# Kernel optimization log

Measured on AMD Instinct MI355X. Metric: run time of the kernel, lower is better.

## Reference

```python
import jax, jax.numpy as jnp
import numpy as np

N = 100000      # nodes
E = 1200000     # edges
D_IN = 128      # input_dim
H = 64          # hidden_dim
OUT = 3         # output_dim
EPS = 1e-5      # BatchNorm eps


def setup_inputs() -> dict:
    key = jax.random.key(0)
    ks = jax.random.split(key, 24)
    w = lambda k, shape: jax.random.normal(k, shape, jnp.float32) * 0.05
    return {
        "x": jax.random.normal(ks[0], (N, D_IN), jnp.float32),
        "edge_index": jax.random.randint(ks[1], (2, E), 0, N, dtype=jnp.int32),
        "proj_W": w(ks[2], (H, D_IN)), "proj_b": w(ks[3], (H,)),
        "conv1_W": w(ks[4], (H, H)), "conv1_b": w(ks[5], (H,)),
        "bn1_g": jnp.ones((H,), jnp.float32), "bn1_b": w(ks[6], (H,)),
        "conv2_W": w(ks[7], (H, H)), "conv2_b": w(ks[8], (H,)),
        "bn2_g": jnp.ones((H,), jnp.float32), "bn2_b": w(ks[9], (H,)),
        "conv3_W": w(ks[10], (H, H)), "conv3_b": w(ks[11], (H,)),
        "bn3_g": jnp.ones((H,), jnp.float32), "bn3_b": w(ks[12], (H,)),
        "byp_W": w(ks[13], (OUT, D_IN)), "byp_b": w(ks[14], (OUT,)),
        "head_W": w(ks[15], (OUT, H + OUT)), "head_b": w(ks[16], (OUT,)),
    }


def reference(x, edge_index, proj_W, proj_b,
              conv1_W, conv1_b, bn1_g, bn1_b,
              conv2_W, conv2_b, bn2_g, bn2_b,
              conv3_W, conv3_b, bn3_g, bn3_b,
              byp_W, byp_b, head_W, head_b):
    n = x.shape[0]
    row, col = edge_index[0], edge_index[1]
    loop = jnp.arange(n, dtype=row.dtype)
    row_f = jnp.concatenate([row, loop])   # source (with self loops)
    col_f = jnp.concatenate([col, loop])   # target
    # symmetric GCN normalization: deg over targets of A+I, edge weight 1
    deg = jax.ops.segment_sum(jnp.ones(row_f.shape, jnp.float32), col_f, num_segments=n)
    dinv = jnp.where(deg > 0, jax.lax.rsqrt(deg), 0.0)
    norm = dinv[row_f] * dinv[col_f]       # [E+N]

    def gcn(h, W, b):
        h = h @ W.T                                    # transform then propagate
        msg = h[row_f] * norm[:, None]                 # gather + scale
        return jax.ops.segment_sum(msg, col_f, num_segments=n) + b

    def bn(h, g, b):
        # eval-mode BatchNorm1d: running_mean=0, running_var=1 buffers
        return h * (g / jnp.sqrt(1.0 + EPS)) + b

    h = x @ proj_W.T + proj_b
    idn = h
    h = jax.nn.relu(bn(gcn(h, conv1_W, conv1_b), bn1_g, bn1_b)) + idn  # dropout inactive (eval)
    idn = h
    h = jax.nn.relu(bn(gcn(h, conv2_W, conv2_b), bn2_g, bn2_b)) + idn
    h = jax.nn.relu(bn(gcn(h, conv3_W, conv3_b), bn3_g, bn3_b))

    byp = x @ byp_W.T + byp_b
    p = jnp.concatenate([h, byp], axis=1) @ head_W.T + head_b
    kappa = jnp.clip(p[:, 0] * 5.0 + 2.5, 0.2, 10.0)
    alpha = p[:, 1]
    tau = jnp.clip(p[:, 2] + 0.5, 0.05, 2.0)
    return jnp.stack([kappa, alpha, tau], axis=1)
```

## Files before the change

kernel.cpp:

```cpp
#include <hip/hip_runtime.h>
#include <hip/hip_fp16.h>

#define NN 100000
#define NE 1200000
#define NBUK ((NN + 127) / 128)
#define NCHUNK 512

typedef _Float16 h8 __attribute__((ext_vector_type(8)));
typedef float f32x4 __attribute__((ext_vector_type(4)));
typedef float f32x2 __attribute__((ext_vector_type(2)));

__global__ __launch_bounds__(256) void k_bucketA(const int* __restrict__ col,
                                                 int* __restrict__ blkcnt,
                                                 int* __restrict__ bcnt) {
    __shared__ int lh[NBUK];
    const int tid = threadIdx.x;
    const int per = (NE + NCHUNK - 1) / NCHUNK;
    const int e0 = blockIdx.x * per;
    const int e1 = (e0 + per < NE) ? (e0 + per) : NE;
    for (int i = tid; i < NBUK; i += 256) lh[i] = 0;
    __syncthreads();
    for (int e = e0 + tid; e < e1; e += 256)
        atomicAdd(&lh[col[e] >> 7], 1);
    __syncthreads();
    for (int b = tid; b < NBUK; b += 256) {
        int v = lh[b];
        blkcnt[b * NCHUNK + blockIdx.x] = v;
        if (v) atomicAdd(&bcnt[b], v);
    }
}

__global__ __launch_bounds__(1024) void k_scanAll(int* __restrict__ blkcnt,
                                                  int* __restrict__ bcnt) {
    __shared__ int s[1024];
    const int b = blockIdx.x, tid = threadIdx.x;
    if (b < NBUK) {
        int v = (tid < NCHUNK) ? blkcnt[b * NCHUNK + tid] : 0;
        s[tid] = v;
        __syncthreads();
        #pragma unroll
        for (int d = 1; d < 1024; d <<= 1) {
            int t = (tid >= d) ? s[tid - d] : 0;
            __syncthreads();
            s[tid] += t;
            __syncthreads();
        }
        if (tid < NCHUNK) blkcnt[b * NCHUNK + tid] = s[tid] - v;
    } else {
        int v = (tid < NBUK) ? bcnt[tid] : 0;
        s[tid] = v;
        __syncthreads();
        #pragma unroll
        for (int d = 1; d < 1024; d <<= 1) {
            int t = (tid >= d) ? s[tid - d] : 0;
            __syncthreads();
            s[tid] += t;
            __syncthreads();
        }
        if (tid < NBUK) bcnt[tid] = s[tid] - v;
        if (tid == 0) bcnt[NBUK] = NE;
    }
}

__global__ __launch_bounds__(256) void k_bucketB(const int* __restrict__ row,
                                                 const int* __restrict__ col,
                                                 const int* __restrict__ bbase,
                                                 const int* __restrict__ blkcnt,
                                                 unsigned* __restrict__ tmp) {
    __shared__ int lh[NBUK];
    const int tid = threadIdx.x;
    const int per = (NE + NCHUNK - 1) / NCHUNK;
    const int e0 = blockIdx.x * per;
    const int e1 = (e0 + per < NE) ? (e0 + per) : NE;
    for (int b = tid; b < NBUK; b += 256)
        lh[b] = bbase[b] + blkcnt[b * NCHUNK + blockIdx.x];
    __syncthreads();
    for (int e = e0 + tid; e < e1; e += 256) {
        int c = col[e], r = row[e];
        int pos = atomicAdd(&lh[c >> 7], 1);
        tmp[pos] = ((unsigned)r << 7) | (unsigned)(c & 127);
    }
}

__global__ __launch_bounds__(256) void k_build(const unsigned* __restrict__ tmp,
                                               const int* __restrict__ bbase,
                                               int* __restrict__ off,
                                               float* __restrict__ dinv,
                                               int* __restrict__ csr_row) {
    __shared__ int cnt[128], s[128], cur[128];
    const int b = blockIdx.x, tid = threadIdx.x;
    const int colBase = b << 7;
    const int nCols = (NN - colBase < 128) ? (NN - colBase) : 128;
    const int seg0 = bbase[b], seg1 = bbase[b + 1];
    if (tid < 128) cnt[tid] = 0;
    __syncthreads();
    for (int i = seg0 + tid; i < seg1; i += 256)
        atomicAdd(&cnt[tmp[i] & 127], 1);
    __syncthreads();
    if (tid < 128) s[tid] = cnt[tid];
    __syncthreads();
    #pragma unroll
    for (int d = 1; d < 128; d <<= 1) {
        int t = (tid < 128 && tid >= d) ? s[tid - d] : 0;
        __syncthreads();
        if (tid < 128) s[tid] += t;
        __syncthreads();
    }
    if (tid < nCols) {
        int exc = seg0 + s[tid] - cnt[tid];
        off[colBase + tid] = exc;
        cur[tid] = exc;
        dinv[colBase + tid] = rsqrtf((float)cnt[tid] + 1.0f);
    }
    if (b == 0 && tid == 0) off[NN] = NE;
    __syncthreads();
    for (int i = seg0 + tid; i < seg1; i += 256) {
        unsigned v = tmp[i];
        int pos = atomicAdd(&cur[v & 127u], 1);
        csr_row[pos] = (int)(v >> 7);
    }
}

__global__ __launch_bounds__(256) void k_gemmPC(const float* __restrict__ X,
                                                const float* __restrict__ W,
                                                const float* __restrict__ bias,
                                                _Float16* __restrict__ Yh,
                                                const float* __restrict__ bypW,
                                                const float* __restrict__ bypb,
                                                float* __restrict__ bypOut,
                                                const float* __restrict__ convW1,
                                                const float* __restrict__ dinv,
                                                unsigned char* __restrict__ Y8,
                                                int n_nodes) {
    constexpr int D = 128, RS = D + 8, KS = D / 32;
    constexpr int RS2 = 72;
    __shared__ _Float16 Xh[64 * RS];
    __shared__ _Float16 Wh[64 * RS];
    const int tid = threadIdx.x;
    const int n0 = blockIdx.x * 64;

    for (int i = tid; i < 64 * (D / 8); i += 256) {
        int j = i / (D / 8), d8 = (i % (D / 8)) * 8;
        const float4* wp = (const float4*)&W[j * D + d8];
        float4 w0 = wp[0], w1 = wp[1];
        h8 h = { (_Float16)w0.x, (_Float16)w0.y, (_Float16)w0.z, (_Float16)w0.w,
                 (_Float16)w1.x, (_Float16)w1.y, (_Float16)w1.z, (_Float16)w1.w };
        *(h8*)&Wh[j * RS + d8] = h;
    }
    for (int i = tid; i < 64 * (D / 8); i += 256) {
        int nl = i / (D / 8), d8 = (i % (D / 8)) * 8;
        int n = n0 + nl; if (n >= n_nodes) n = n_nodes - 1;
        const float4* xp = (const float4*)&X[(size_t)n * D + d8];
        float4 x0 = xp[0], x1 = xp[1];
        h8 h = { (_Float16)x0.x, (_Float16)x0.y, (_Float16)x0.z, (_Float16)x0.w,
                 (_Float16)x1.x, (_Float16)x1.y, (_Float16)x1.z, (_Float16)x1.w };
        *(h8*)&Xh[nl * RS + d8] = h;
    }
    __syncthreads();

    const int wid = tid >> 6, lane = tid & 63;
    const int lm = lane & 15, lq = lane >> 4;
    const int mBase = wid * 16;

    h8 bfrag[4][KS];
    #pragma unroll
    for (int t = 0; t < 4; ++t)
        #pragma unroll
        for (int s = 0; s < KS; ++s)
            bfrag[t][s] = *(const h8*)&Wh[(t * 16 + lm) * RS + s * 32 + lq * 8];

    h8 bfragB[KS];
    #pragma unroll
    for (int s = 0; s < KS; ++s) {
        if (lm < 3) {
            const float4* wp = (const float4*)&bypW[lm * D + s * 32 + lq * 8];
            float4 w0 = wp[0], w1 = wp[1];
            bfragB[s] = (h8){ (_Float16)w0.x, (_Float16)w0.y, (_Float16)w0.z, (_Float16)w0.w,
                              (_Float16)w1.x, (_Float16)w1.y, (_Float16)w1.z, (_Float16)w1.w };
        } else {
            bfragB[s] = (h8)(_Float16)0;
        }
    }

    f32x4 acc[5] = {};
    #pragma unroll
    for (int s = 0; s < KS; ++s) {
        h8 a = *(const h8*)&Xh[(mBase + lm) * RS + s * 32 + lq * 8];
        #pragma unroll
        for (int t = 0; t < 4; ++t)
            acc[t] = __builtin_amdgcn_mfma_f32_16x16x32_f16(a, bfrag[t][s], acc[t], 0, 0, 0);
        acc[4] = __builtin_amdgcn_mfma_f32_16x16x32_f16(a, bfragB[s], acc[4], 0, 0, 0);
    }

    float bb[4];
    #pragma unroll
    for (int t = 0; t < 4; ++t) bb[t] = bias[t * 16 + lm];
    float bypbv = (lm < 3) ? bypb[lm] : 0.f;
    const int nodeBase = n0 + mBase + lq * 4;

    __syncthreads();

    #pragma unroll
    for (int r = 0; r < 4; ++r) {
        int node = nodeBase + r;
        int nloc = mBase + lq * 4 + r;
        #pragma unroll
        for (int t = 0; t < 4; ++t) {
            _Float16 hv = (_Float16)(acc[t][r] + bb[t]);
            Xh[nloc * RS2 + t * 16 + lm] = hv;
            if (node < n_nodes)
                Yh[(size_t)node * 64 + t * 16 + lm] = hv;
        }
        if (node < n_nodes && lm < 3)
            bypOut[node * 3 + lm] = acc[4][r] + bypbv;
    }
    for (int i = tid; i < 64 * 8; i += 256) {
        int j = i >> 3, d8 = (i & 7) * 8;
        const float4* wp = (const float4*)&convW1[j * 64 + d8];
        float4 w0 = wp[0], w1 = wp[1];
        h8 h = { (_Float16)w0.x, (_Float16)w0.y, (_Float16)w0.z, (_Float16)w0.w,
                 (_Float16)w1.x, (_Float16)w1.y, (_Float16)w1.z, (_Float16)w1.w };
        *(h8*)&Wh[j * RS2 + d8] = h;
    }
    __syncthreads();

    h8 cfrag[4][2];
    #pragma unroll
    for (int t = 0; t < 4; ++t)
        #pragma unroll
        for (int s = 0; s < 2; ++s)
            cfrag[t][s] = *(const h8*)&Wh[(t * 16 + lm) * RS2 + s * 32 + lq * 8];

    f32x4 acc2[4] = {};
    #pragma unroll
    for (int s = 0; s < 2; ++s) {
        h8 a = *(const h8*)&Xh[(mBase + lm) * RS2 + s * 32 + lq * 8];
        #pragma unroll
        for (int t = 0; t < 4; ++t)
            acc2[t] = __builtin_amdgcn_mfma_f32_16x16x32_f16(a, cfrag[t][s], acc2[t], 0, 0, 0);
    }
    #pragma unroll
    for (int r = 0; r < 4; ++r) {
        int node = nodeBase + r;
        if (node < n_nodes) {
            float sdv = dinv[node];
            #pragma unroll
            for (int t = 0; t < 4; ++t) {
                float v = acc2[t][r] * sdv;
                int pk = __builtin_amdgcn_cvt_pk_fp8_f32(v, v, 0, false);
                Y8[(size_t)node * 64 + t * 16 + lm] = (unsigned char)(pk & 0xff);
            }
        }
    }
}

__device__ __forceinline__ void acc_fp8(float* acc, uint2 w) {
    f32x2 p0 = __builtin_amdgcn_cvt_pk_f32_fp8(w.x, false);
    f32x2 p1 = __builtin_amdgcn_cvt_pk_f32_fp8(w.x, true);
    f32x2 p2 = __builtin_amdgcn_cvt_pk_f32_fp8(w.y, false);
    f32x2 p3 = __builtin_amdgcn_cvt_pk_f32_fp8(w.y, true);
    acc[0] += p0.x; acc[1] += p0.y; acc[2] += p1.x; acc[3] += p1.y;
    acc[4] += p2.x; acc[5] += p2.y; acc[6] += p3.x; acc[7] += p3.y;
}

template<bool HEAD>
__global__ __launch_bounds__(256) void k_gather(const unsigned char* __restrict__ hB8,
                                                const float* __restrict__ dinv,
                                                const int* __restrict__ off,
                                                const int* __restrict__ csr_row,
                                                const float* __restrict__ convb,
                                                const float* __restrict__ bng,
                                                const float* __restrict__ bnb,
                                                _Float16* __restrict__ hA,
                                                const float* __restrict__ nextW,
                                                unsigned char* __restrict__ Y8,
                                                const float* __restrict__ byp,
                                                const float* __restrict__ headW,
                                                const float* __restrict__ headb,
                                                float* __restrict__ out) {
    constexpr int RS2 = 72;
    __shared__ _Float16 Ws[HEAD ? 1 : 64 * RS2];
    __shared__ _Float16 Hs[HEAD ? 1 : 32 * RS2];
    __shared__ float HWs[HEAD ? 204 : 1];
    const int tid = threadIdx.x;
    if constexpr (HEAD) {
        for (int i = tid; i < 204; i += 256)
            HWs[i] = (i < 201) ? headW[i] : headb[i - 201];
        __syncthreads();
    } else {
        for (int i = tid; i < 64 * 8; i += 256) {
            int j = i >> 3, d8 = (i & 7) * 8;
            const float4* wp = (const float4*)&nextW[j * 64 + d8];
            float4 w0 = wp[0], w1 = wp[1];
            h8 h = { (_Float16)w0.x, (_Float16)w0.y, (_Float16)w0.z, (_Float16)w0.w,
                     (_Float16)w1.x, (_Float16)w1.y, (_Float16)w1.z, (_Float16)w1.w };
            *(h8*)&Ws[j * RS2 + d8] = h;
        }
    }
    const int wid = tid >> 6, lane = tid & 63;
    const int nloc = wid * 8 + (lane >> 3);
    const int n = blockIdx.x * 32 + nloc;
    const int oct = lane & 7;
    const int f0 = oct * 8;

    const int e0 = off[n];
    const int deg = off[n + 1] - e0;

    const uint2* rows8 = (const uint2*)hB8;
    float acc[8] = {0, 0, 0, 0, 0, 0, 0, 0};
    acc_fp8(acc, rows8[(size_t)n * 8 + oct]);

    for (int it = 0; it < deg; it += 8) {
        const int rem = deg - it;
        uint2 w[8];
        #pragma unroll
        for (int q = 0; q < 8; ++q) {
            int rq = csr_row[e0 + it + ((q < rem) ? q : 0)];
            w[q] = rows8[(size_t)rq * 8 + oct];
            if (q >= rem) { w[q].x = 0; w[q].y = 0; }
        }
        #pragma unroll
        for (int q = 0; q < 8; ++q)
            acc_fp8(acc, w[q]);
    }

    const float dv = dinv[n];
    const float bnscale = rsqrtf(1.0f + 1e-5f);
    const float4 cb0 = *(const float4*)&convb[f0], cb1 = *(const float4*)&convb[f0 + 4];
    const float4 g0  = *(const float4*)&bng[f0],  g1  = *(const float4*)&bng[f0 + 4];
    const float4 b0_ = *(const float4*)&bnb[f0],  b1_ = *(const float4*)&bnb[f0 + 4];
    const float cb[8] = { cb0.x, cb0.y, cb0.z, cb0.w, cb1.x, cb1.y, cb1.z, cb1.w };
    const float gg[8] = { g0.x, g0.y, g0.z, g0.w, g1.x, g1.y, g1.z, g1.w };
    const float bb[8] = { b0_.x, b0_.y, b0_.z, b0_.w, b1_.x, b1_.y, b1_.z, b1_.w };
    float v[8];
    #pragma unroll
    for (int j = 0; j < 8; ++j)
        v[j] = fmaxf((acc[j] * dv + cb[j]) * (gg[j] * bnscale) + bb[j], 0.0f);

    if constexpr (!HEAD) {
        size_t o = ((size_t)n << 6) + f0;
        h8 old = *(const h8*)&hA[o];
        #pragma unroll
        for (int j = 0; j < 8; ++j) v[j] += (float)old[j];
        h8 res = { (_Float16)v[0], (_Float16)v[1], (_Float16)v[2], (_Float16)v[3],
                   (_Float16)v[4], (_Float16)v[5], (_Float16)v[6], (_Float16)v[7] };
        *(h8*)&hA[o] = res;
        *(h8*)&Hs[nloc * RS2 + f0] = res;
        __syncthreads();

        const int lm = lane & 15, lq = lane >> 4;
        const int mt = (wid & 1) * 16;
        const int nt = (wid >> 1) * 32;
        h8 afrag[2], bfrag[2][2];
        #pragma unroll
        for (int s = 0; s < 2; ++s)
            afrag[s] = *(const h8*)&Hs[(mt + lm) * RS2 + s * 32 + lq * 8];
        #pragma unroll
        for (int t = 0; t < 2; ++t)
            #pragma unroll
            for (int s = 0; s < 2; ++s)
                bfrag[t][s] = *(const h8*)&Ws[(nt + t * 16 + lm) * RS2 + s * 32 + lq * 8];
        f32x4 acc2[2] = {};
        #pragma unroll
        for (int s = 0; s < 2; ++s)
            #pragma unroll
            for (int t = 0; t < 2; ++t)
                acc2[t] = __builtin_amdgcn_mfma_f32_16x16x32_f16(afrag[s], bfrag[t][s], acc2[t], 0, 0, 0);
        const int nodeBase = blockIdx.x * 32 + mt + lq * 4;
        #pragma unroll
        for (int r = 0; r < 4; ++r) {
            int node = nodeBase + r;
            float sdv = dinv[node];
            #pragma unroll
            for (int t = 0; t < 2; ++t) {
                float vv = acc2[t][r] * sdv;
                int pk = __builtin_amdgcn_cvt_pk_fp8_f32(vv, vv, 0, false);
                Y8[(size_t)node * 64 + nt + t * 16 + lm] = (unsigned char)(pk & 0xff);
            }
        }
    } else {
        float p[3];
        #pragma unroll
        for (int o = 0; o < 3; ++o) {
            float t = 0.f;
            #pragma unroll
            for (int j = 0; j < 8; ++j) t += v[j] * HWs[o * 67 + f0 + j];
            p[o] = t;
        }
        #pragma unroll
        for (int mask = 1; mask < 8; mask <<= 1) {
            #pragma unroll
            for (int o = 0; o < 3; ++o) p[o] += __shfl_xor(p[o], mask, 64);
        }
        if (oct == 0) {
            float by0 = byp[n * 3], by1 = byp[n * 3 + 1], by2 = byp[n * 3 + 2];
            #pragma unroll
            for (int o = 0; o < 3; ++o)
                p[o] += by0 * HWs[o * 67 + 64] + by1 * HWs[o * 67 + 65] + by2 * HWs[o * 67 + 66]
                      + HWs[201 + o];
            float kappa = fminf(fmaxf(p[0] * 5.0f + 2.5f, 0.2f), 10.0f);
            float tau   = fminf(fmaxf(p[2] + 0.5f, 0.05f), 2.0f);
            out[(size_t)n * 3]     = kappa;
            out[(size_t)n * 3 + 1] = p[1];
            out[(size_t)n * 3 + 2] = tau;
        }
    }
}

extern "C" void kernel_launch(void* const* d_in, const int* in_sizes, int n_in,
                              void* d_out, int out_size, void* d_ws, size_t ws_size,
                              hipStream_t stream) {
    const float* x     = (const float*)d_in[0];
    const int*   ei    = (const int*)d_in[1];
    const int*   row   = ei;
    const int*   col   = ei + NE;
    const float* projW = (const float*)d_in[2];
    const float* projb = (const float*)d_in[3];
    const float* convW[3] = { (const float*)d_in[4], (const float*)d_in[8],  (const float*)d_in[12] };
    const float* convb[3] = { (const float*)d_in[5], (const float*)d_in[9],  (const float*)d_in[13] };
    const float* bng[3]   = { (const float*)d_in[6], (const float*)d_in[10], (const float*)d_in[14] };
    const float* bnb[3]   = { (const float*)d_in[7], (const float*)d_in[11], (const float*)d_in[15] };
    const float* bypW  = (const float*)d_in[16];
    const float* bypb  = (const float*)d_in[17];
    const float* headW = (const float*)d_in[18];
    const float* headb = (const float*)d_in[19];
    float* out = (float*)d_out;

    float*    ws   = (float*)d_ws;
    float*    dinv = ws;
    _Float16* hAh  = (_Float16*)(ws + 102400);
    unsigned char* hB8a = (unsigned char*)(hAh + (size_t)NN * 64);
    float*    byp  = (float*)(hB8a + (size_t)NN * 64);
    int*      off     = (int*)(byp + 300032);
    int*      csr_row = off + 100096;
    int*      bcnt    = csr_row + NE;
    int*      blkcnt  = bcnt + 784;
    unsigned char* hB8b = (unsigned char*)(blkcnt + (size_t)NBUK * NCHUNK);
    unsigned* tmp     = (unsigned*)hAh;

    hipMemsetAsync(bcnt, 0, 784 * sizeof(int), stream);
    k_bucketA<<<NCHUNK, 256, 0, stream>>>(col, blkcnt, bcnt);
    k_scanAll<<<NBUK + 1, 1024, 0, stream>>>(blkcnt, bcnt);
    k_bucketB<<<NCHUNK, 256, 0, stream>>>(row, col, bcnt, blkcnt, tmp);
    k_build<<<NBUK, 256, 0, stream>>>(tmp, bcnt, off, dinv, csr_row);

    k_gemmPC<<<(NN + 63) / 64, 256, 0, stream>>>(
        x, projW, projb, hAh, bypW, bypb, byp, convW[0], dinv, hB8a, NN);

    k_gather<false><<<NN / 32, 256, 0, stream>>>(
        hB8a, dinv, off, csr_row, convb[0], bng[0], bnb[0], hAh,
        convW[1], hB8b, nullptr, nullptr, nullptr, nullptr);
    k_gather<false><<<NN / 32, 256, 0, stream>>>(
        hB8b, dinv, off, csr_row, convb[1], bng[1], bnb[1], hAh,
        convW[2], hB8a, nullptr, nullptr, nullptr, nullptr);
    k_gather<true><<<NN / 32, 256, 0, stream>>>(
        hB8a, dinv, off, csr_row, convb[2], bng[2], bnb[2], nullptr,
        nullptr, nullptr, byp, headW, headb, out);
}
```

Measured before the change: 258.2 us.

## Gather fp8 rows with 4 lanes per node using 32-byte loads and edge split

Restructures the sparse gather so each node is handled by 4 lanes instead of 8. Each lane loads 32 bytes (half a 64-byte fp8 row) from every second edge, and the two edge halves are combined with a shuffle. Blocks now cover 64 nodes, and each wave runs the follow-on 16x64 MFMA transform for its own 16 nodes. The goal is fewer, wider memory requests and more edge-level parallelism per lane. In exchange each lane holds 32 float accumulators, which raises register pressure and may lower occupancy.

```diff
diff --git a/kernel.cpp b/kernel.cpp
--- a/kernel.cpp
+++ b/kernel.cpp
@@ -254,13 +254,15 @@
     }
 }
 
-__device__ __forceinline__ void acc_fp8(float* acc, uint2 w) {
-    f32x2 p0 = __builtin_amdgcn_cvt_pk_f32_fp8(w.x, false);
-    f32x2 p1 = __builtin_amdgcn_cvt_pk_f32_fp8(w.x, true);
-    f32x2 p2 = __builtin_amdgcn_cvt_pk_f32_fp8(w.y, false);
-    f32x2 p3 = __builtin_amdgcn_cvt_pk_f32_fp8(w.y, true);
-    acc[0] += p0.x; acc[1] += p0.y; acc[2] += p1.x; acc[3] += p1.y;
-    acc[4] += p2.x; acc[5] += p2.y; acc[6] += p3.x; acc[7] += p3.y;
+__device__ __forceinline__ void acc32(float* acc, uint4 a, uint4 b) {
+    unsigned u[8] = {a.x, a.y, a.z, a.w, b.x, b.y, b.z, b.w};
+    #pragma unroll
+    for (int k = 0; k < 8; ++k) {
+        f32x2 lo = __builtin_amdgcn_cvt_pk_f32_fp8(u[k], false);
+        f32x2 hi = __builtin_amdgcn_cvt_pk_f32_fp8(u[k], true);
+        acc[k * 4]     += lo.x; acc[k * 4 + 1] += lo.y;
+        acc[k * 4 + 2] += hi.x; acc[k * 4 + 3] += hi.y;
+    }
 }
 
 template<bool HEAD>
@@ -280,7 +282,7 @@
                                                 float* __restrict__ out) {
     constexpr int RS2 = 72;
     __shared__ _Float16 Ws[HEAD ? 1 : 64 * RS2];
-    __shared__ _Float16 Hs[HEAD ? 1 : 32 * RS2];
+    __shared__ _Float16 Hs[HEAD ? 1 : 64 * RS2];
     __shared__ float HWs[HEAD ? 204 : 1];
     const int tid = threadIdx.x;
     if constexpr (HEAD) {
@@ -298,101 +300,134 @@
         }
     }
     const int wid = tid >> 6, lane = tid & 63;
-    const int nloc = wid * 8 + (lane >> 3);
-    const int n = blockIdx.x * 32 + nloc;
-    const int oct = lane & 7;
-    const int f0 = oct * 8;
-
-    const int e0 = off[n];
-    const int deg = off[n + 1] - e0;
-
-    const uint2* rows8 = (const uint2*)hB8;
-    float acc[8] = {0, 0, 0, 0, 0, 0, 0, 0};
-    acc_fp8(acc, rows8[(size_t)n * 8 + oct]);
-
-    for (int it = 0; it < deg; it += 8) {
-        const int rem = deg - it;
-        uint2 w[8];
-        #pragma unroll
-        for (int q = 0; q < 8; ++q) {
-            int rq = csr_row[e0 + it + ((q < rem) ? q : 0)];
-            w[q] = rows8[(size_t)rq * 8 + oct];
-            if (q >= rem) { w[q].x = 0; w[q].y = 0; }
-        }
-        #pragma unroll
-        for (int q = 0; q < 8; ++q)
-            acc_fp8(acc, w[q]);
-    }
-
-    const float dv = dinv[n];
+    const int bb = blockIdx.x * 64;
+    const int nloc = wid * 16 + (lane >> 2);
+    const int n = bb + nloc;
+    const int sub = lane & 3;
+    const int fh = sub & 1;
+    const int es = sub >> 1;
+    const bool act = n < NN;
+
+    const uint4* rows16 = (const uint4*)hB8;
+    float acc[32];
+    #pragma unroll
+    for (int k = 0; k < 32; ++k) acc[k] = 0.f;
+    int e0 = 0, deg = 0;
+    if (act) {
+        e0 = off[n]; deg = off[n + 1] - e0;
+        if (es == 0) {
+            uint4 s0 = rows16[(size_t)n * 4 + fh * 2];
+            uint4 s1 = rows16[(size_t)n * 4 + fh * 2 + 1];
+            acc32(acc, s0, s1);
+        }
+    }
+    for (int base = 0; base < deg; base += 8) {
+        uint4 wa[4], wb[4];
+        #pragma unroll
+        for (int q = 0; q < 4; ++q) {
+            int eix = base + 2 * q + es;
+            if (eix < deg) {
+                int rq = csr_row[e0 + eix];
+                wa[q] = rows16[(size_t)rq * 4 + fh * 2];
+                wb[q] = rows16[(size_t)rq * 4 + fh * 2 + 1];
+            } else {
+                wa[q] = make_uint4(0, 0, 0, 0);
+                wb[q] = make_uint4(0, 0, 0, 0);
+            }
+        }
+        #pragma unroll
+        for (int q = 0; q < 4; ++q) acc32(acc, wa[q], wb[q]);
+    }
+
+    const int ko = es * 16;
+    const int fb = fh * 32 + ko;
+    float vq[16];
+    #pragma unroll
+    for (int j = 0; j < 16; ++j) {
+        float other = __shfl_xor(acc[(ko ^ 16) + j], 2, 64);
+        vq[j] = acc[ko + j] + other;
+    }
+
     const float bnscale = rsqrtf(1.0f + 1e-5f);
-    const float4 cb0 = *(const float4*)&convb[f0], cb1 = *(const float4*)&convb[f0 + 4];
-    const float4 g0  = *(const float4*)&bng[f0],  g1  = *(const float4*)&bng[f0 + 4];
-    const float4 b0_ = *(const float4*)&bnb[f0],  b1_ = *(const float4*)&bnb[f0 + 4];
-    const float cb[8] = { cb0.x, cb0.y, cb0.z, cb0.w, cb1.x, cb1.y, cb1.z, cb1.w };
-    const float gg[8] = { g0.x, g0.y, g0.z, g0.w, g1.x, g1.y, g1.z, g1.w };
-    const float bb[8] = { b0_.x, b0_.y, b0_.z, b0_.w, b1_.x, b1_.y, b1_.z, b1_.w };
-    float v[8];
-    #pragma unroll
-    for (int j = 0; j < 8; ++j)
-        v[j] = fmaxf((acc[j] * dv + cb[j]) * (gg[j] * bnscale) + bb[j], 0.0f);
+    float dv = act ? dinv[n] : 0.f;
+    float cc[16], GG[16], BB[16];
+    #pragma unroll
+    for (int j4 = 0; j4 < 4; ++j4) {
+        float4 c = *(const float4*)&convb[fb + j4 * 4];
+        float4 g = *(const float4*)&bng[fb + j4 * 4];
+        float4 b = *(const float4*)&bnb[fb + j4 * 4];
+        cc[j4 * 4] = c.x; cc[j4 * 4 + 1] = c.y; cc[j4 * 4 + 2] = c.z; cc[j4 * 4 + 3] = c.w;
+        GG[j4 * 4] = g.x; GG[j4 * 4 + 1] = g.y; GG[j4 * 4 + 2] = g.z; GG[j4 * 4 + 3] = g.w;
+        BB[j4 * 4] = b.x; BB[j4 * 4 + 1] = b.y; BB[j4 * 4 + 2] = b.z; BB[j4 * 4 + 3] = b.w;
+    }
+    float v[16];
+    #pragma unroll
+    for (int j = 0; j < 16; ++j)
+        v[j] = fmaxf((vq[j] * dv + cc[j]) * (GG[j] * bnscale) + BB[j], 0.0f);
 
     if constexpr (!HEAD) {
-        size_t o = ((size_t)n << 6) + f0;
-        h8 old = *(const h8*)&hA[o];
-        #pragma unroll
-        for (int j = 0; j < 8; ++j) v[j] += (float)old[j];
-        h8 res = { (_Float16)v[0], (_Float16)v[1], (_Float16)v[2], (_Float16)v[3],
-                   (_Float16)v[4], (_Float16)v[5], (_Float16)v[6], (_Float16)v[7] };
-        *(h8*)&hA[o] = res;
-        *(h8*)&Hs[nloc * RS2 + f0] = res;
+        if (act) {
+            size_t o = ((size_t)n << 6) + fb;
+            h8 old0 = *(const h8*)&hA[o];
+            h8 old1 = *(const h8*)&hA[o + 8];
+            h8 r0, r1;
+            #pragma unroll
+            for (int j = 0; j < 8; ++j) {
+                r0[j] = (_Float16)(v[j] + (float)old0[j]);
+                r1[j] = (_Float16)(v[8 + j] + (float)old1[j]);
+            }
+            *(h8*)&hA[o] = r0;
+            *(h8*)&hA[o + 8] = r1;
+            *(h8*)&Hs[nloc * RS2 + fb] = r0;
+            *(h8*)&Hs[nloc * RS2 + fb + 8] = r1;
+        }
         __syncthreads();
 
         const int lm = lane & 15, lq = lane >> 4;
-        const int mt = (wid & 1) * 16;
-        const int nt = (wid >> 1) * 32;
-        h8 afrag[2], bfrag[2][2];
-        #pragma unroll
-        for (int s = 0; s < 2; ++s)
-            afrag[s] = *(const h8*)&Hs[(mt + lm) * RS2 + s * 32 + lq * 8];
-        #pragma unroll
-        for (int t = 0; t < 2; ++t)
+        h8 bfrag[4][2];
+        #pragma unroll
+        for (int t4 = 0; t4 < 4; ++t4)
             #pragma unroll
             for (int s = 0; s < 2; ++s)
-                bfrag[t][s] = *(const h8*)&Ws[(nt + t * 16 + lm) * RS2 + s * 32 + lq * 8];
-        f32x4 acc2[2] = {};
+                bfrag[t4][s] = *(const h8*)&Ws[(t4 * 16 + lm) * RS2 + s * 32 + lq * 8];
+        h8 af[2];
+        #pragma unroll
+        for (int s = 0; s < 2; ++s)
+            af[s] = *(const h8*)&Hs[(wid * 16 + lm) * RS2 + s * 32 + lq * 8];
+        f32x4 acc2[4] = {};
         #pragma unroll
         for (int s = 0; s < 2; ++s)
             #pragma unroll
-            for (int t = 0; t < 2; ++t)
-                acc2[t] = __builtin_amdgcn_mfma_f32_16x16x32_f16(afrag[s], bfrag[t][s], acc2[t], 0, 0, 0);
-        const int nodeBase = blockIdx.x * 32 + mt + lq * 4;
+            for (int t4 = 0; t4 < 4; ++t4)
+                acc2[t4] = __builtin_amdgcn_mfma_f32_16x16x32_f16(af[s], bfrag[t4][s], acc2[t4], 0, 0, 0);
+        const int nodeBase = bb + wid * 16 + lq * 4;
         #pragma unroll
         for (int r = 0; r < 4; ++r) {
             int node = nodeBase + r;
-            float sdv = dinv[node];
-            #pragma unroll
-            for (int t = 0; t < 2; ++t) {
-                float vv = acc2[t][r] * sdv;
-                int pk = __builtin_amdgcn_cvt_pk_fp8_f32(vv, vv, 0, false);
-                Y8[(size_t)node * 64 + nt + t * 16 + lm] = (unsigned char)(pk & 0xff);
+            if (node < NN) {
+                float sdv = dinv[node];
+                #pragma unroll
+                for (int t4 = 0; t4 < 4; ++t4) {
+                    float vv = acc2[t4][r] * sdv;
+                    int pk = __builtin_amdgcn_cvt_pk_fp8_f32(vv, vv, 0, false);
+                    Y8[(size_t)node * 64 + t4 * 16 + lm] = (unsigned char)(pk & 0xff);
+                }
             }
         }
     } else {
-        float p[3];
+        float p[3] = {0.f, 0.f, 0.f};
+        #pragma unroll
+        for (int j = 0; j < 16; ++j) {
+            p[0] += v[j] * HWs[0 * 67 + fb + j];
+            p[1] += v[j] * HWs[1 * 67 + fb + j];
+            p[2] += v[j] * HWs[2 * 67 + fb + j];
+        }
         #pragma unroll
         for (int o = 0; o < 3; ++o) {
-            float t = 0.f;
-            #pragma unroll
-            for (int j = 0; j < 8; ++j) t += v[j] * HWs[o * 67 + f0 + j];
-            p[o] = t;
-        }
-        #pragma unroll
-        for (int mask = 1; mask < 8; mask <<= 1) {
-            #pragma unroll
-            for (int o = 0; o < 3; ++o) p[o] += __shfl_xor(p[o], mask, 64);
-        }
-        if (oct == 0) {
+            p[o] += __shfl_xor(p[o], 1, 64);
+            p[o] += __shfl_xor(p[o], 2, 64);
+        }
+        if (act && sub == 0) {
             float by0 = byp[n * 3], by1 = byp[n * 3 + 1], by2 = byp[n * 3 + 2];
             #pragma unroll
             for (int o = 0; o < 3; ++o)
@@ -447,13 +482,13 @@
     k_gemmPC<<<(NN + 63) / 64, 256, 0, stream>>>(
         x, projW, projb, hAh, bypW, bypb, byp, convW[0], dinv, hB8a, NN);
 
-    k_gather<false><<<NN / 32, 256, 0, stream>>>(
+    k_gather<false><<<(NN + 63) / 64, 256, 0, stream>>>(
         hB8a, dinv, off, csr_row, convb[0], bng[0], bnb[0], hAh,
         convW[1], hB8b, nullptr, nullptr, nullptr, nullptr);
-    k_gather<false><<<NN / 32, 256, 0, stream>>>(
+    k_gather<false><<<(NN + 63) / 64, 256, 0, stream>>>(
         hB8b, dinv, off, csr_row, convb[1], bng[1], bnb[1], hAh,
         convW[2], hB8a, nullptr, nullptr, nullptr, nullptr);
-    k_gather<true><<<NN / 32, 256, 0, stream>>>(
+    k_gather<true><<<(NN + 63) / 64, 256, 0, stream>>>(
         hB8a, dinv, off, csr_row, convb[2], bng[2], bnb[2], nullptr,
         nullptr, nullptr, byp, headW, headb, out);
 }
```

Result: slower. 382.4 us (+48.1%).
